# Kernel tuning notes

Hardware: AMD Instinct MI355X
Metric: run time of the kernel (lower is better)

## Reference

```python
import jax, jax.numpy as jnp
import numpy as np

WIN = (2, 2, 8, 8)
NUM_HEADS = 6
DIM = 120
HID = int(DIM * 2.0)
SHAPE = (8, 4, 64, 64, DIM)


def _layernorm(x, w, b, eps=1e-5):
    m = jnp.mean(x, axis=-1, keepdims=True)
    v = jnp.mean((x - m) ** 2, axis=-1, keepdims=True)
    return (x - m) / jnp.sqrt(v + eps) * w + b


def _window_partition(x, win):
    N, D, H, W, C = x.shape
    x = x.reshape(N // win[0], win[0], D // win[1], win[1],
                  H // win[2], win[2], W // win[3], win[3], C)
    x = jnp.transpose(x, (0, 2, 4, 6, 1, 3, 5, 7, 8))
    return x.reshape(-1, win[0] * win[1] * win[2] * win[3], C)


def _window_reverse(wins, win, N, D, H, W):
    x = wins.reshape(N // win[0], D // win[1], H // win[2], W // win[3],
                     win[0], win[1], win[2], win[3], -1)
    x = jnp.transpose(x, (0, 4, 1, 5, 2, 6, 3, 7, 8))
    return x.reshape(N, D, H, W, -1)


def _mha(q, k, v, scale):
    # q,k,v: (B_, h, n, hd) -> (B_, n, h*hd)
    a = jax.nn.softmax(jnp.einsum('bhid,bhjd->bhij', q * scale, k), axis=-1)
    o = jnp.einsum('bhij,bhjd->bhid', a, v)
    B, h, n, hd = o.shape
    return jnp.transpose(o, (0, 2, 1, 3)).reshape(B, n, h * hd)


def _qkv(xw, W, b, heads):
    B, n, C = xw.shape
    qkv = (xw @ W.T + b).reshape(B, n, 3, heads, C // heads)
    qkv = jnp.transpose(qkv, (2, 0, 3, 1, 4))
    return qkv[0], qkv[1], qkv[2]


def _tmsa(x, norm1_w, norm1_b, qkv_self_w, qkv_self_b, qkv_mut_w, qkv_mut_b,
          proj_w, proj_b, norm2_w, norm2_b, fc11_w, fc11_b, fc12_w, fc12_b,
          fc2_w, fc2_b):
    N, D, H, W, C = x.shape
    heads = NUM_HEADS
    scale = (C // heads) ** -0.5
    # --- attention branch (no shift -> no roll, no mask; dims divide window -> no pad) ---
    h = _layernorm(x, norm1_w, norm1_b)
    xw = _window_partition(h, WIN)                       # (B_, n, C)
    q, k, v = _qkv(xw, qkv_self_w, qkv_self_b, heads)
    x_self = _mha(q, k, v, scale)                        # (B_, n, C)
    q, k, v = _qkv(xw, qkv_mut_w, qkv_mut_b, heads)
    n = xw.shape[1]
    q1, q2 = q[:, :, :n // 2], q[:, :, n // 2:]
    k1, k2 = k[:, :, :n // 2], k[:, :, n // 2:]
    v1, v2 = v[:, :, :n // 2], v[:, :, n // 2:]
    x1 = _mha(q2, k1, v1, scale)                         # (B_, n/2, C)
    x2 = _mha(q1, k2, v2, scale)
    x_mut = jnp.concatenate([x1, x2], axis=1)            # (B_, n, C)
    x_out = jnp.concatenate([x_mut, x_self], axis=2)     # (B_, n, 2C)
    attn = x_out @ proj_w.T + proj_b                     # (B_, n, C)
    attn = _window_reverse(attn, WIN, N, D, H, W)
    x = x + attn
    # --- GEGLU MLP branch ---
    h2 = _layernorm(x, norm2_w, norm2_b)
    gate = jax.nn.gelu(h2 @ fc11_w.T + fc11_b, approximate=False)
    hid = gate * (h2 @ fc12_w.T + fc12_b)
    x = x + (hid @ fc2_w.T + fc2_b)
    return x


def setup_inputs() -> dict:
    key = jax.random.key(0)
    ks = jax.random.split(key, 8)
    s = 0.02
    return {
        'x': jax.random.normal(ks[0], SHAPE, dtype=jnp.float32),
        'norm1_w': jnp.ones((DIM,), jnp.float32),
        'norm1_b': jnp.zeros((DIM,), jnp.float32),
        'qkv_self_w': jax.random.normal(ks[1], (3 * DIM, DIM), jnp.float32) * s,
        'qkv_self_b': jnp.zeros((3 * DIM,), jnp.float32),
        'qkv_mut_w': jax.random.normal(ks[2], (3 * DIM, DIM), jnp.float32) * s,
        'qkv_mut_b': jnp.zeros((3 * DIM,), jnp.float32),
        'proj_w': jax.random.normal(ks[3], (DIM, 2 * DIM), jnp.float32) * s,
        'proj_b': jnp.zeros((DIM,), jnp.float32),
        'norm2_w': jnp.ones((DIM,), jnp.float32),
        'norm2_b': jnp.zeros((DIM,), jnp.float32),
        'fc11_w': jax.random.normal(ks[4], (HID, DIM), jnp.float32) * s,
        'fc11_b': jnp.zeros((HID,), jnp.float32),
        'fc12_w': jax.random.normal(ks[5], (HID, DIM), jnp.float32) * s,
        'fc12_b': jnp.zeros((HID,), jnp.float32),
        'fc2_w': jax.random.normal(ks[6], (DIM, HID), jnp.float32) * s,
        'fc2_b': jnp.zeros((DIM,), jnp.float32),
    }


def reference(x, norm1_w, norm1_b, qkv_self_w, qkv_self_b, qkv_mut_w,
              qkv_mut_b, proj_w, proj_b, norm2_w, norm2_b, fc11_w, fc11_b,
              fc12_w, fc12_b, fc2_w, fc2_b):
    return _tmsa(x, norm1_w, norm1_b, qkv_self_w, qkv_self_b, qkv_mut_w,
                 qkv_mut_b, proj_w, proj_b, norm2_w, norm2_b, fc11_w, fc11_b,
                 fc12_w, fc12_b, fc2_w, fc2_b)
```

## Files before the change

### kernel.cpp

```cpp
#include <hip/hip_runtime.h>
#include <hip/hip_bf16.h>
#include <math.h>


typedef __attribute__((ext_vector_type(8))) short bf16x8;
typedef __attribute__((ext_vector_type(4))) float f32x4;

#define SCALE2 (0.22360679774997896f * 1.44269504088896340f)
#define CHROWS 65536
#define QPLANE 7864320u

union B8U { bf16x8 v; uint4 u4; uint2 u2[2]; unsigned u[4]; short s[8]; };

__device__ __forceinline__ short bf16b(float f) {
    __hip_bfloat16 h = __float2bfloat16(f);
    return *reinterpret_cast<short*>(&h);
}
__device__ __forceinline__ float bf2f(short s) {
    return __uint_as_float(((unsigned)(unsigned short)s) << 16);
}
__device__ __forceinline__ unsigned packbf(float a, float b) {
    return (unsigned)(unsigned short)bf16b(a) |
           ((unsigned)(unsigned short)bf16b(b) << 16);
}

__device__ __forceinline__ int rev_row(int r) {
    int w = r >> 8, t = r & 255;
    int w8 = w & 7, h8 = (w >> 3) & 7, d2 = (w >> 6) & 1, n2 = w >> 7;
    int www = t & 7, hh = (t >> 3) & 7, dd = (t >> 6) & 1, nn = t >> 7;
    int n = n2 * 2 + nn, d = d2 * 2 + dd;
    int Hc = h8 * 8 + hh, Wc = w8 * 8 + www;
    return ((n * 4 + d) << 12) + (Hc << 6) + Wc;
}
__device__ __forceinline__ int part_row(int g) {
    int ww = g & 63, hh = (g >> 6) & 63, d = (g >> 12) & 3, n = g >> 14;
    int w = ((n >> 1) * 2 + (d >> 1)) * 64 + ((hh >> 3) << 3) + (ww >> 3);
    int t = (((n & 1) * 2 + (d & 1)) << 6) + ((hh & 7) << 3) + (ww & 7);
    return (w << 8) + t;
}
__device__ __forceinline__ float gelu_exact(float x) {
    return 0.5f * x * (1.0f + erff(x * 0.70710678118654752f));
}

__device__ __forceinline__ bf16x8 load_frag20(const short* row, int quad) {
    B8U r;
    const uint2* p = (const uint2*)(row + quad * 8);
    r.u2[0] = p[0]; r.u2[1] = p[1];
    if (quad == 2) { r.u[2] = 0; r.u[3] = 0; }
    else if (quad == 3) { r.u[0] = r.u[1] = r.u[2] = r.u[3] = 0; }
    return r.v;
}

__device__ __forceinline__ void stageA_frag(uint4* Af, const short* __restrict__ A,
                                            int bm, int k0, int Astr, int tid) {
#pragma unroll
    for (int i = 0; i < 8; ++i) {
        int c = i * 256 + tid;
        int row = c >> 4, q = c & 15;
        uint4 v = make_uint4(0u, 0u, 0u, 0u);
        if (q < 15) v = *(const uint4*)(A + (size_t)(bm + row) * Astr + k0 + q * 8);
        Af[((row >> 4) * 4 + (q >> 2)) * 64 + (q & 3) * 16 + (row & 15)] = v;
    }
}
__device__ __forceinline__ void stageW_frag(uint4* Wf, const float* __restrict__ W,
                                            int bn, int k0, int Wstr, int N, int tid) {
#pragma unroll
    for (int i = 0; i < 4; ++i) {
        int c = i * 256 + tid;
        int row = c >> 4, q = c & 15;
        int wr = bn + row; if (wr > N - 1) wr = N - 1;
        uint4 d = make_uint4(0u, 0u, 0u, 0u);
        if (q < 15) {
            f32x4 w0 = *(const f32x4*)(W + (size_t)wr * Wstr + k0 + q * 8);
            f32x4 w1 = *(const f32x4*)(W + (size_t)wr * Wstr + k0 + q * 8 + 4);
            d = make_uint4(packbf(w0.x, w0.y), packbf(w0.z, w0.w),
                           packbf(w1.x, w1.y), packbf(w1.z, w1.w));
        }
        Wf[((row >> 4) * 4 + (q >> 2)) * 64 + (q & 3) * 16 + (row & 15)] = d;
    }
}

template <bool REMAP>
__global__ __launch_bounds__(256) void ln_kernel(const float* __restrict__ in,
                                                 const float* __restrict__ w,
                                                 const float* __restrict__ b,
                                                 short* __restrict__ out) {
    int row  = blockIdx.x * 4 + (threadIdx.x >> 6);
    int lane = threadIdx.x & 63;
    const float* xr = in + (size_t)row * 120;
    float2 v = make_float2(0.f, 0.f);
    if (lane < 60) v = *(const float2*)(xr + lane * 2);
    float s = v.x + v.y;
#pragma unroll
    for (int off = 32; off; off >>= 1) s += __shfl_down(s, off, 64);
    s = __shfl(s, 0, 64);
    float mean = s * (1.f / 120.f);
    float dx = v.x - mean, dy = v.y - mean;
    float q = (lane < 60) ? (dx * dx + dy * dy) : 0.f;
#pragma unroll
    for (int off = 32; off; off >>= 1) q += __shfl_down(q, off, 64);
    q = __shfl(q, 0, 64);
    float rstd = rsqrtf(q * (1.f / 120.f) + 1e-5f);
    int orow = REMAP ? part_row(row) : row;
    if (lane < 60) {
        float2 wv = *(const float2*)(w + lane * 2);
        float2 bv = *(const float2*)(b + lane * 2);
        unsigned u = packbf(dx * rstd * wv.x + bv.x, dy * rstd * wv.y + bv.y);
        *(unsigned*)(out + (size_t)orow * 120 + lane * 2) = u;
    }
}

template <int MODE, int K, int N>
__global__ __launch_bounds__(256) void mm(const short* __restrict__ A,
                                          const float* __restrict__ W,
                                          const float* __restrict__ bias,
                                          void* __restrict__ outp,
                                          const float* __restrict__ aux,
                                          int m0) {
    __shared__ uint4 Af[2048];
    __shared__ uint4 Wf[1024];
    const int tid = threadIdx.x;
    const int lane = tid & 63, wave = tid >> 6;
    const int quad = lane >> 4, l16 = lane & 15;
    const int bmb = blockIdx.x * 128;
    const int bn  = blockIdx.y * 64;
    const int atile = (wave >> 1) * 4;
    const int wtile = (wave & 1) * 2;

    f32x4 acc[4][2];
#pragma unroll
    for (int i = 0; i < 4; ++i)
#pragma unroll
        for (int j = 0; j < 2; ++j) acc[i][j] = (f32x4){0.f, 0.f, 0.f, 0.f};

    constexpr int PH = K / 120;
#pragma unroll
    for (int p = 0; p < PH; ++p) {
        if (p) __syncthreads();
        stageA_frag(Af, A, bmb, p * 120, K, tid);
        stageW_frag(Wf, W, bn, p * 120, K, N, tid);
        __syncthreads();
#pragma unroll
        for (int kt = 0; kt < 4; ++kt) {
            B8U b0, b1;
            b0.u4 = Wf[((wtile + 0) * 4 + kt) * 64 + lane];
            b1.u4 = Wf[((wtile + 1) * 4 + kt) * 64 + lane];
#pragma unroll
            for (int i = 0; i < 4; ++i) {
                B8U a; a.u4 = Af[((atile + i) * 4 + kt) * 64 + lane];
                acc[i][0] = __builtin_amdgcn_mfma_f32_16x16x32_bf16(a.v, b0.v, acc[i][0], 0, 0, 0);
                acc[i][1] = __builtin_amdgcn_mfma_f32_16x16x32_bf16(a.v, b1.v, acc[i][1], 0, 0, 0);
            }
        }
    }

    const int bm = bmb + atile * 16;
#pragma unroll
    for (int j = 0; j < 2; ++j) {
        const int n = bn + wtile * 16 + j * 16 + l16;
        if (n >= N) continue;
        const float bs = bias[n];
        int which = 0, head = 0, e = 0;
        if (MODE == 0) { which = n / 120; int hn = n % 120; head = hn / 20; e = hn % 20; }
#pragma unroll
        for (int i = 0; i < 4; ++i) {
#pragma unroll
            for (int r = 0; r < 4; ++r) {
                int m = bm + i * 16 + quad * 4 + r;
                float val = acc[i][j][r] + bs;
                if (MODE == 0) {
                    if (which == 0) val *= SCALE2;
                    int wl = m >> 8, t = m & 255;
                    ((short*)outp)[(size_t)which * QPLANE +
                                   ((size_t)((wl * 6 + head) * 256 + t)) * 20 + e] = bf16b(val);
                } else if (MODE == 1) {
                    int g = rev_row(m0 + m);
                    val += aux[(size_t)g * 120 + n];
                    ((float*)outp)[(size_t)(m0 + m) * 120 + n] = val;
                } else {
                    int g = rev_row(m0 + m);
                    val += aux[(size_t)m * 120 + n];
                    ((float*)outp)[(size_t)g * 120 + n] = val;
                }
            }
        }
    }
}

__global__ __launch_bounds__(256) void mm_mlp(const short* __restrict__ A,
                                              const float* __restrict__ W1,
                                              const float* __restrict__ b1,
                                              const float* __restrict__ W2,
                                              const float* __restrict__ b2,
                                              short* __restrict__ outp) {
    __shared__ uint4 Af[2048];
    __shared__ uint4 Wf[1024];
    const int tid = threadIdx.x;
    const int lane = tid & 63, wave = tid >> 6;
    const int quad = lane >> 4, l16 = lane & 15;
    const int bmb = blockIdx.x * 128;
    const int bn  = blockIdx.y * 64;
    const int atile = (wave >> 1) * 4;
    const int wtile = (wave & 1) * 2;
    const int N = 240;

    f32x4 acc1[4][2], acc2[4][2];
#pragma unroll
    for (int i = 0; i < 4; ++i)
#pragma unroll
        for (int j = 0; j < 2; ++j) {
            acc1[i][j] = (f32x4){0.f, 0.f, 0.f, 0.f};
            acc2[i][j] = (f32x4){0.f, 0.f, 0.f, 0.f};
        }

    stageA_frag(Af, A, bmb, 0, 120, tid);
    stageW_frag(Wf, W1, bn, 0, 120, N, tid);
    __syncthreads();
#pragma unroll
    for (int kt = 0; kt < 4; ++kt) {
        B8U b0, b1;
        b0.u4 = Wf[((wtile + 0) * 4 + kt) * 64 + lane];
        b1.u4 = Wf[((wtile + 1) * 4 + kt) * 64 + lane];
#pragma unroll
        for (int i = 0; i < 4; ++i) {
            B8U a; a.u4 = Af[((atile + i) * 4 + kt) * 64 + lane];
            acc1[i][0] = __builtin_amdgcn_mfma_f32_16x16x32_bf16(a.v, b0.v, acc1[i][0], 0, 0, 0);
            acc1[i][1] = __builtin_amdgcn_mfma_f32_16x16x32_bf16(a.v, b1.v, acc1[i][1], 0, 0, 0);
        }
    }
    __syncthreads();
    stageW_frag(Wf, W2, bn, 0, 120, N, tid);
    __syncthreads();
#pragma unroll
    for (int kt = 0; kt < 4; ++kt) {
        B8U b0, b1;
        b0.u4 = Wf[((wtile + 0) * 4 + kt) * 64 + lane];
        b1.u4 = Wf[((wtile + 1) * 4 + kt) * 64 + lane];
#pragma unroll
        for (int i = 0; i < 4; ++i) {
            B8U a; a.u4 = Af[((atile + i) * 4 + kt) * 64 + lane];
            acc2[i][0] = __builtin_amdgcn_mfma_f32_16x16x32_bf16(a.v, b0.v, acc2[i][0], 0, 0, 0);
            acc2[i][1] = __builtin_amdgcn_mfma_f32_16x16x32_bf16(a.v, b1.v, acc2[i][1], 0, 0, 0);
        }
    }

    const int bm = bmb + atile * 16;
#pragma unroll
    for (int j = 0; j < 2; ++j) {
        const int n = bn + wtile * 16 + j * 16 + l16;
        if (n >= N) continue;
        const float g1 = b1[n], g2 = b2[n];
#pragma unroll
        for (int i = 0; i < 4; ++i) {
#pragma unroll
            for (int r = 0; r < 4; ++r) {
                int m = bm + i * 16 + quad * 4 + r;
                float gv = acc1[i][j][r] + g1;
                float vv = acc2[i][j][r] + g2;
                outp[(size_t)m * 240 + n] = bf16b(gelu_exact(gv) * vv);
            }
        }
    }
}

template <int NK, bool MUT>
__global__ __launch_bounds__(NK) void attn_flash(const short* __restrict__ qkv,
                                                 short* __restrict__ xout) {
    constexpr int NKT = NK / 32;
    constexpr int VSTR2 = NK + 4;
    __shared__ __align__(16) short Kf[NKT * 2 * 48 * 8];
    __shared__ __align__(16) unsigned Vt2[11 * VSTR2];
    const int b = blockIdx.x;
    int wl, hd, half;
    if (MUT) { half = b & 1; hd = (b >> 1) % 6; wl = b / 12; }
    else     { half = 0;     hd = b % 6;        wl = b / 6;  }
    const int tid  = threadIdx.x;
    const int lane = tid & 63, wave = tid >> 6;
    const int quad = lane >> 4, l16 = lane & 15;

    const size_t rb = (size_t)(wl * 6 + hd) * 256;
    const short* qpl = qkv + rb * 20;
    const short* kpl = qkv + (size_t)QPLANE + rb * 20;
    const short* vpl = qkv + 2 * (size_t)QPLANE + rb * 20;
    const int koff = MUT ? half * 128 : 0;
    const int qoff = MUT ? (1 - half) * 128 : 0;

    {
        const uint2* p = (const uint2*)(vpl + (size_t)(koff + tid) * 20);
        unsigned tmp[10];
#pragma unroll
        for (int i = 0; i < 5; ++i) ((uint2*)tmp)[i] = p[i];
#pragma unroll
        for (int i = 0; i < 10; ++i) Vt2[i * VSTR2 + tid] = tmp[i];
        Vt2[10 * VSTR2 + tid] = 0x00003F80u;

        int skt = tid >> 5, sf = (tid >> 4) & 1, sl = tid & 15;
        int srow = koff + skt * 32 + sf * 4 + ((sl >> 2) << 3) + (sl & 3);
        const uint2* kp = (const uint2*)(kpl + (size_t)srow * 20);
        uint2 k0 = kp[0], k1 = kp[1], k2 = kp[2], k3 = kp[3], k4 = kp[4];
        uint4* dst = (uint4*)Kf + ((skt * 2 + sf) * 48 + sl);
        dst[0]  = make_uint4(k0.x, k0.y, k1.x, k1.y);
        dst[16] = make_uint4(k2.x, k2.y, k3.x, k3.y);
        dst[32] = make_uint4(k4.x, k4.y, 0u, 0u);
    }
    __syncthreads();

    const int quadc = quad < 3 ? quad : 2;
    const uint4* kfrag = (const uint4*)Kf + quadc * 16 + l16;
    const unsigned sel = (l16 & 1) ? 0x07060302u : 0x05040100u;
    const unsigned* vbase0 = Vt2 + (l16 >> 1) * VSTR2;
    int r1 = 8 + (l16 >> 1); if (r1 > 10) r1 = 10;
    const unsigned* vbase1 = Vt2 + r1 * VSTR2;
    const f32x4 z4 = {0.f, 0.f, 0.f, 0.f};

#pragma unroll 1
    for (int g = 0; g < 2; ++g) {
        bf16x8 bq0 = load_frag20(qpl + (size_t)(qoff + wave * 64 + (g * 2 + 0) * 16 + l16) * 20, quad);
        bf16x8 bq1 = load_frag20(qpl + (size_t)(qoff + wave * 64 + (g * 2 + 1) * 16 + l16) * 20, quad);

        f32x4 accO[2][2];
        accO[0][0] = z4; accO[0][1] = z4; accO[1][0] = z4; accO[1][1] = z4;

#pragma unroll
        for (int kt = 0; kt < NKT; ++kt) {
            B8U ak0, ak1;
            ak0.u4 = kfrag[(kt * 2 + 0) * 48];
            ak1.u4 = kfrag[(kt * 2 + 1) * 48];
            B8U av0, av1;
            {
                uint4 va = *(const uint4*)(vbase0 + kt * 32 + quad * 8);
                uint4 vb = *(const uint4*)(vbase0 + kt * 32 + quad * 8 + 4);
                av0.u[0] = __builtin_amdgcn_perm(va.y, va.x, sel);
                av0.u[1] = __builtin_amdgcn_perm(va.w, va.z, sel);
                av0.u[2] = __builtin_amdgcn_perm(vb.y, vb.x, sel);
                av0.u[3] = __builtin_amdgcn_perm(vb.w, vb.z, sel);
                uint4 vc = *(const uint4*)(vbase1 + kt * 32 + quad * 8);
                uint4 vd = *(const uint4*)(vbase1 + kt * 32 + quad * 8 + 4);
                av1.u[0] = __builtin_amdgcn_perm(vc.y, vc.x, sel);
                av1.u[1] = __builtin_amdgcn_perm(vc.w, vc.z, sel);
                av1.u[2] = __builtin_amdgcn_perm(vd.y, vd.x, sel);
                av1.u[3] = __builtin_amdgcn_perm(vd.w, vd.z, sel);
            }
#pragma unroll
            for (int t = 0; t < 2; ++t) {
                bf16x8 bqt = t ? bq1 : bq0;
                f32x4 s0 = __builtin_amdgcn_mfma_f32_16x16x32_bf16(ak0.v, bqt, z4, 0, 0, 0);
                f32x4 s1 = __builtin_amdgcn_mfma_f32_16x16x32_bf16(ak1.v, bqt, z4, 0, 0, 0);
                float p0 = __builtin_amdgcn_exp2f(s0[0]), p1 = __builtin_amdgcn_exp2f(s0[1]);
                float p2 = __builtin_amdgcn_exp2f(s0[2]), p3 = __builtin_amdgcn_exp2f(s0[3]);
                float p4 = __builtin_amdgcn_exp2f(s1[0]), p5 = __builtin_amdgcn_exp2f(s1[1]);
                float p6 = __builtin_amdgcn_exp2f(s1[2]), p7 = __builtin_amdgcn_exp2f(s1[3]);
                B8U bp;
                bp.u[0] = packbf(p0, p1);
                bp.u[1] = packbf(p2, p3);
                bp.u[2] = packbf(p4, p5);
                bp.u[3] = packbf(p6, p7);
                accO[t][0] = __builtin_amdgcn_mfma_f32_16x16x32_bf16(av0.v, bp.v, accO[t][0], 0, 0, 0);
                accO[t][1] = __builtin_amdgcn_mfma_f32_16x16x32_bf16(av1.v, bp.v, accO[t][1], 0, 0, 0);
            }
        }

#pragma unroll
        for (int t = 0; t < 2; ++t) {
            int nt = g * 2 + t;
            float l = __shfl(accO[t][1][0], 16 + l16, 64);
            float inv = 1.f / l;
            int tok = (MUT ? half * 128 : 0) + wave * 64 + nt * 16 + l16;
            short* orow = xout + (size_t)(wl * 256 + tok) * 240 + (MUT ? hd * 20 : 120 + hd * 20);
            unsigned lo = packbf(accO[t][0][0] * inv, accO[t][0][1] * inv);
            unsigned hi2 = packbf(accO[t][0][2] * inv, accO[t][0][3] * inv);
            *(uint2*)(orow + quad * 4) = make_uint2(lo, hi2);
            if (quad == 0) {
                unsigned lo2 = packbf(accO[t][1][0] * inv, accO[t][1][1] * inv);
                unsigned hi3 = packbf(accO[t][1][2] * inv, accO[t][1][3] * inv);
                *(uint2*)(orow + 16) = make_uint2(lo2, hi3);
            }
        }
    }
}

extern "C" void kernel_launch(void* const* d_in, const int* in_sizes, int n_in,
                              void* d_out, int out_size, void* d_ws, size_t ws_size,
                              hipStream_t stream) {
    const float* x          = (const float*)d_in[0];
    const float* norm1_w    = (const float*)d_in[1];
    const float* norm1_b    = (const float*)d_in[2];
    const float* qkv_self_w = (const float*)d_in[3];
    const float* qkv_self_b = (const float*)d_in[4];
    const float* qkv_mut_w  = (const float*)d_in[5];
    const float* qkv_mut_b  = (const float*)d_in[6];
    const float* proj_w     = (const float*)d_in[7];
    const float* proj_b     = (const float*)d_in[8];
    const float* norm2_w    = (const float*)d_in[9];
    const float* norm2_b    = (const float*)d_in[10];
    const float* fc11_w     = (const float*)d_in[11];
    const float* fc11_b     = (const float*)d_in[12];
    const float* fc12_w     = (const float*)d_in[13];
    const float* fc12_b     = (const float*)d_in[14];
    const float* fc2_w      = (const float*)d_in[15];
    const float* fc2_b      = (const float*)d_in[16];

    if (ws_size < 110100480u) return;

    char* wsb   = (char*)d_ws;
    short* Hb    = (short*)wsb;
    short* QKVc  = (short*)(wsb + 31457280);
    short* XOUTc = (short*)(wsb + 78643200);
    float* TMP   = (float*)wsb;
    short* H2c   = (short*)(wsb + 62914560);
    short* HIDc  = (short*)(wsb + 78643200);
    float* X2    = (float*)d_out;
    float* out   = (float*)d_out;

    ln_kernel<true><<<32768, 256, 0, stream>>>(x, norm1_w, norm1_b, Hb);

    for (int c = 0; c < 2; ++c) {
        int m0 = c * CHROWS;
        const short* Ac = Hb + (size_t)m0 * 120;
        mm<0, 120, 360><<<dim3(512, 6), 256, 0, stream>>>(Ac, qkv_self_w, qkv_self_b,
                                                          QKVc, nullptr, 0);
        attn_flash<256, false><<<1536, 256, 0, stream>>>(QKVc, XOUTc);
        mm<0, 120, 360><<<dim3(512, 6), 256, 0, stream>>>(Ac, qkv_mut_w, qkv_mut_b,
                                                          QKVc, nullptr, 0);
        attn_flash<128, true><<<3072, 128, 0, stream>>>(QKVc, XOUTc);
        mm<1, 240, 120><<<dim3(512, 2), 256, 0, stream>>>(XOUTc, proj_w, proj_b,
                                                          X2, x, m0);
    }

    hipMemcpyAsync(TMP, d_out, 62914560u, hipMemcpyDeviceToDevice, stream);

    for (int c = 0; c < 2; ++c) {
        int m0 = c * CHROWS;
        ln_kernel<false><<<16384, 256, 0, stream>>>(TMP + (size_t)m0 * 120,
                                                    norm2_w, norm2_b, H2c);
        mm_mlp<<<dim3(512, 4), 256, 0, stream>>>(H2c, fc11_w, fc11_b,
                                                 fc12_w, fc12_b, HIDc);
        mm<4, 240, 120><<<dim3(512, 2), 256, 0, stream>>>(HIDc, fc2_w, fc2_b,
                                                          out, TMP + (size_t)m0 * 120, m0);
    }
}
```

Baseline: 623.2 us.

## Load GEMM A fragments directly from global and swizzle LDS weight tiles

The GEMM kernels stop staging the activation tile through shared memory. Each wave now reads its bf16 A fragments straight from global memory into registers, and only the converted weight tile is staged in LDS, in a single pass over the full K, with an XOR swizzle meant to cut bank conflicts. The fused MLP kernel stages both weight matrices up front and runs both GEMMs in one loop with a single barrier. This removes LDS traffic and barriers, but A reads become strided, and the two waves that share the same rows load them twice, so the kernel relies on caches.

```diff
diff --git a/kernel.cpp b/kernel.cpp
--- a/kernel.cpp
+++ b/kernel.cpp
@@ -23,6 +23,8 @@
     return (unsigned)(unsigned short)bf16b(a) |
            ((unsigned)(unsigned short)bf16b(b) << 16);
 }
+
+__device__ __forceinline__ int swz(int idx) { return idx ^ ((idx >> 4) & 7); }
 
 __device__ __forceinline__ int rev_row(int r) {
     int w = r >> 8, t = r & 255;
@@ -51,32 +53,25 @@
     return r.v;
 }
 
-__device__ __forceinline__ void stageA_frag(uint4* Af, const short* __restrict__ A,
-                                            int bm, int k0, int Astr, int tid) {
-#pragma unroll
-    for (int i = 0; i < 8; ++i) {
+template <int K>
+__device__ __forceinline__ void stageW_frag(uint4* Wf, const float* __restrict__ W,
+                                            int bn, int N, int tid) {
+    constexpr int CH   = (K == 120) ? 16 : 32;
+    constexpr int NKT  = CH / 4;
+    constexpr int ITER = 64 * CH / 256;
+#pragma unroll
+    for (int i = 0; i < ITER; ++i) {
         int c = i * 256 + tid;
-        int row = c >> 4, q = c & 15;
-        uint4 v = make_uint4(0u, 0u, 0u, 0u);
-        if (q < 15) v = *(const uint4*)(A + (size_t)(bm + row) * Astr + k0 + q * 8);
-        Af[((row >> 4) * 4 + (q >> 2)) * 64 + (q & 3) * 16 + (row & 15)] = v;
-    }
-}
-__device__ __forceinline__ void stageW_frag(uint4* Wf, const float* __restrict__ W,
-                                            int bn, int k0, int Wstr, int N, int tid) {
-#pragma unroll
-    for (int i = 0; i < 4; ++i) {
-        int c = i * 256 + tid;
-        int row = c >> 4, q = c & 15;
+        int row = c / CH, q = c % CH;
         int wr = bn + row; if (wr > N - 1) wr = N - 1;
         uint4 d = make_uint4(0u, 0u, 0u, 0u);
-        if (q < 15) {
-            f32x4 w0 = *(const f32x4*)(W + (size_t)wr * Wstr + k0 + q * 8);
-            f32x4 w1 = *(const f32x4*)(W + (size_t)wr * Wstr + k0 + q * 8 + 4);
+        if (q * 8 < K) {
+            f32x4 w0 = *(const f32x4*)(W + (size_t)wr * K + q * 8);
+            f32x4 w1 = *(const f32x4*)(W + (size_t)wr * K + q * 8 + 4);
             d = make_uint4(packbf(w0.x, w0.y), packbf(w0.z, w0.w),
                            packbf(w1.x, w1.y), packbf(w1.z, w1.w));
         }
-        Wf[((row >> 4) * 4 + (q >> 2)) * 64 + (q & 3) * 16 + (row & 15)] = d;
+        Wf[swz(((row >> 4) * NKT + (q >> 2)) * 64 + (q & 3) * 16 + (row & 15))] = d;
     }
 }
 
@@ -117,47 +112,46 @@
                                           void* __restrict__ outp,
                                           const float* __restrict__ aux,
                                           int m0) {
-    __shared__ uint4 Af[2048];
-    __shared__ uint4 Wf[1024];
+    constexpr int NKT = (K + 31) / 32;
+    __shared__ uint4 Wf[4 * NKT * 64];
     const int tid = threadIdx.x;
     const int lane = tid & 63, wave = tid >> 6;
     const int quad = lane >> 4, l16 = lane & 15;
-    const int bmb = blockIdx.x * 128;
-    const int bn  = blockIdx.y * 64;
-    const int atile = (wave >> 1) * 4;
+    const int bm  = blockIdx.x * 128 + (wave >> 1) * 64;
+    const int bnb = blockIdx.y * 64;
     const int wtile = (wave & 1) * 2;
 
+    stageW_frag<K>(Wf, W, bnb, N, tid);
+
+    const short* Ar[4];
+#pragma unroll
+    for (int i = 0; i < 4; ++i) Ar[i] = A + (size_t)(bm + i * 16 + l16) * K;
+
     f32x4 acc[4][2];
 #pragma unroll
     for (int i = 0; i < 4; ++i)
 #pragma unroll
         for (int j = 0; j < 2; ++j) acc[i][j] = (f32x4){0.f, 0.f, 0.f, 0.f};
 
-    constexpr int PH = K / 120;
-#pragma unroll
-    for (int p = 0; p < PH; ++p) {
-        if (p) __syncthreads();
-        stageA_frag(Af, A, bmb, p * 120, K, tid);
-        stageW_frag(Wf, W, bn, p * 120, K, N, tid);
-        __syncthreads();
-#pragma unroll
-        for (int kt = 0; kt < 4; ++kt) {
-            B8U b0, b1;
-            b0.u4 = Wf[((wtile + 0) * 4 + kt) * 64 + lane];
-            b1.u4 = Wf[((wtile + 1) * 4 + kt) * 64 + lane];
-#pragma unroll
-            for (int i = 0; i < 4; ++i) {
-                B8U a; a.u4 = Af[((atile + i) * 4 + kt) * 64 + lane];
-                acc[i][0] = __builtin_amdgcn_mfma_f32_16x16x32_bf16(a.v, b0.v, acc[i][0], 0, 0, 0);
-                acc[i][1] = __builtin_amdgcn_mfma_f32_16x16x32_bf16(a.v, b1.v, acc[i][1], 0, 0, 0);
-            }
-        }
-    }
-
-    const int bm = bmb + atile * 16;
+    __syncthreads();
+#pragma unroll
+    for (int kt = 0; kt < NKT; ++kt) {
+        int k = kt * 32 + quad * 8;
+        int kc = (k + 8 <= K) ? k : 0;
+        B8U b0, b1;
+        b0.u4 = Wf[swz(((wtile + 0) * NKT + kt) * 64 + lane)];
+        b1.u4 = Wf[swz(((wtile + 1) * NKT + kt) * 64 + lane)];
+#pragma unroll
+        for (int i = 0; i < 4; ++i) {
+            bf16x8 a = *(const bf16x8*)(Ar[i] + kc);
+            acc[i][0] = __builtin_amdgcn_mfma_f32_16x16x32_bf16(a, b0.v, acc[i][0], 0, 0, 0);
+            acc[i][1] = __builtin_amdgcn_mfma_f32_16x16x32_bf16(a, b1.v, acc[i][1], 0, 0, 0);
+        }
+    }
+
 #pragma unroll
     for (int j = 0; j < 2; ++j) {
-        const int n = bn + wtile * 16 + j * 16 + l16;
+        const int n = bnb + wtile * 16 + j * 16 + l16;
         if (n >= N) continue;
         const float bs = bias[n];
         int which = 0, head = 0, e = 0;
@@ -193,16 +187,21 @@
                                               const float* __restrict__ W2,
                                               const float* __restrict__ b2,
                                               short* __restrict__ outp) {
-    __shared__ uint4 Af[2048];
-    __shared__ uint4 Wf[1024];
+    __shared__ uint4 Wf[2][4 * 4 * 64];
     const int tid = threadIdx.x;
     const int lane = tid & 63, wave = tid >> 6;
     const int quad = lane >> 4, l16 = lane & 15;
-    const int bmb = blockIdx.x * 128;
-    const int bn  = blockIdx.y * 64;
-    const int atile = (wave >> 1) * 4;
+    const int bm  = blockIdx.x * 128 + (wave >> 1) * 64;
+    const int bnb = blockIdx.y * 64;
     const int wtile = (wave & 1) * 2;
     const int N = 240;
+
+    stageW_frag<120>(Wf[0], W1, bnb, N, tid);
+    stageW_frag<120>(Wf[1], W2, bnb, N, tid);
+
+    const short* Ar[4];
+#pragma unroll
+    for (int i = 0; i < 4; ++i) Ar[i] = A + (size_t)(bm + i * 16 + l16) * 120;
 
     f32x4 acc1[4][2], acc2[4][2];
 #pragma unroll
@@ -213,41 +212,29 @@
             acc2[i][j] = (f32x4){0.f, 0.f, 0.f, 0.f};
         }
 
-    stageA_frag(Af, A, bmb, 0, 120, tid);
-    stageW_frag(Wf, W1, bn, 0, 120, N, tid);
     __syncthreads();
 #pragma unroll
     for (int kt = 0; kt < 4; ++kt) {
-        B8U b0, b1;
-        b0.u4 = Wf[((wtile + 0) * 4 + kt) * 64 + lane];
-        b1.u4 = Wf[((wtile + 1) * 4 + kt) * 64 + lane];
+        int k = kt * 32 + quad * 8;
+        int kc = (k + 8 <= 120) ? k : 0;
+        B8U p0, p1, q0, q1;
+        p0.u4 = Wf[0][swz(((wtile + 0) * 4 + kt) * 64 + lane)];
+        p1.u4 = Wf[0][swz(((wtile + 1) * 4 + kt) * 64 + lane)];
+        q0.u4 = Wf[1][swz(((wtile + 0) * 4 + kt) * 64 + lane)];
+        q1.u4 = Wf[1][swz(((wtile + 1) * 4 + kt) * 64 + lane)];
 #pragma unroll
         for (int i = 0; i < 4; ++i) {
-            B8U a; a.u4 = Af[((atile + i) * 4 + kt) * 64 + lane];
-            acc1[i][0] = __builtin_amdgcn_mfma_f32_16x16x32_bf16(a.v, b0.v, acc1[i][0], 0, 0, 0);
-            acc1[i][1] = __builtin_amdgcn_mfma_f32_16x16x32_bf16(a.v, b1.v, acc1[i][1], 0, 0, 0);
-        }
-    }
-    __syncthreads();
-    stageW_frag(Wf, W2, bn, 0, 120, N, tid);
-    __syncthreads();
-#pragma unroll
-    for (int kt = 0; kt < 4; ++kt) {
-        B8U b0, b1;
-        b0.u4 = Wf[((wtile + 0) * 4 + kt) * 64 + lane];
-        b1.u4 = Wf[((wtile + 1) * 4 + kt) * 64 + lane];
-#pragma unroll
-        for (int i = 0; i < 4; ++i) {
-            B8U a; a.u4 = Af[((atile + i) * 4 + kt) * 64 + lane];
-            acc2[i][0] = __builtin_amdgcn_mfma_f32_16x16x32_bf16(a.v, b0.v, acc2[i][0], 0, 0, 0);
-            acc2[i][1] = __builtin_amdgcn_mfma_f32_16x16x32_bf16(a.v, b1.v, acc2[i][1], 0, 0, 0);
-        }
-    }
-
-    const int bm = bmb + atile * 16;
+            bf16x8 a = *(const bf16x8*)(Ar[i] + kc);
+            acc1[i][0] = __builtin_amdgcn_mfma_f32_16x16x32_bf16(a, p0.v, acc1[i][0], 0, 0, 0);
+            acc1[i][1] = __builtin_amdgcn_mfma_f32_16x16x32_bf16(a, p1.v, acc1[i][1], 0, 0, 0);
+            acc2[i][0] = __builtin_amdgcn_mfma_f32_16x16x32_bf16(a, q0.v, acc2[i][0], 0, 0, 0);
+            acc2[i][1] = __builtin_amdgcn_mfma_f32_16x16x32_bf16(a, q1.v, acc2[i][1], 0, 0, 0);
+        }
+    }
+
 #pragma unroll
     for (int j = 0; j < 2; ++j) {
-        const int n = bn + wtile * 16 + j * 16 + l16;
+        const int n = bnb + wtile * 16 + j * 16 + l16;
         if (n >= N) continue;
         const float g1 = b1[n], g2 = b2[n];
 #pragma unroll
```

After: 612.0 us. Within noise of the previous version (-1.8%).
